# Performance work log

Measured on AMD Instinct MI355X. Metric: run time of the kernel, lower is better.

The kernel has to match this reference:

```python
import jax, jax.numpy as jnp
import numpy as np

EPS = 1e-6
HEADS = 16

def _ln(x):
    m = jnp.mean(x, axis=-1, keepdims=True)
    v = jnp.mean((x - m) ** 2, axis=-1, keepdims=True)
    return (x - m) / jnp.sqrt(v + EPS)

def _modulate(x, shift, scale):
    # shift/scale: [B,T,D] broadcast over H,W
    return x * (1.0 + scale[:, :, None, None, :]) + shift[:, :, None, None, :]

def _gate(x, g):
    return x * g[:, :, None, None, :]

def _mlp(x, w1, b1, w2, b2):
    h = jax.nn.gelu(x @ w1 + b1, approximate=True)
    return h @ w2 + b2

def _attn(tokens, qkv_w, out_w, out_b, causal):
    # tokens: [N, L, D]
    N, L, D = tokens.shape
    dh = D // HEADS
    qkv = tokens @ qkv_w  # [N, L, 3D]
    q, k, v = jnp.split(qkv, 3, axis=-1)
    q = q.reshape(N, L, HEADS, dh)
    k = k.reshape(N, L, HEADS, dh)
    v = v.reshape(N, L, HEADS, dh)
    scores = jnp.einsum('nqhd,nkhd->nhqk', q, k) * (1.0 / np.sqrt(dh))
    if causal:
        mask = jnp.tril(jnp.ones((L, L), dtype=bool))
        scores = jnp.where(mask, scores, jnp.finfo(scores.dtype).min)
    p = jax.nn.softmax(scores, axis=-1)
    o = jnp.einsum('nhqk,nkhd->nqhd', p, v).reshape(N, L, D)
    return o @ out_w + out_b

def _lstm(xseq, w_ih, w_hh, b_ih, b_hh):
    # xseq: [N, T, D]; PyTorch gate order i,f,g,o; zero initial state
    N = xseq.shape[0]
    Hh = w_hh.shape[0]
    def step(carry, xt):
        h, cc = carry
        gates = xt @ w_ih + h @ w_hh + (b_ih + b_hh)  # [N, 4H]
        i, f, g, o = jnp.split(gates, 4, axis=-1)
        cc = jax.nn.sigmoid(f) * cc + jax.nn.sigmoid(i) * jnp.tanh(g)
        h = jax.nn.sigmoid(o) * jnp.tanh(cc)
        return (h, cc), h
    h0 = jnp.zeros((N, Hh), xseq.dtype)
    (_, _), ys = jax.lax.scan(step, (h0, h0), jnp.swapaxes(xseq, 0, 1))
    return jnp.swapaxes(ys, 0, 1)

def _forward(x, c, s_ada_w, s_ada_b, t_ada_w, t_ada_b, r_ada_w, r_ada_b,
             s_qkv_w, s_out_w, s_out_b, t_qkv_w, t_out_w, t_out_b,
             s_mlp_w1, s_mlp_b1, s_mlp_w2, s_mlp_b2,
             t_mlp_w1, t_mlp_b1, t_mlp_w2, t_mlp_b2,
             lstm_w_ih, lstm_w_hh, lstm_b_ih, lstm_b_hh):
    B, T, H, W, D = x.shape
    cs = jax.nn.silu(c)
    s_mod = jnp.split(cs @ s_ada_w + s_ada_b, 6, axis=-1)
    s_shift_msa, s_scale_msa, s_gate_msa, s_shift_mlp, s_scale_mlp, s_gate_mlp = s_mod
    # spatial attention over (H*W) tokens, per (B,T)
    h1 = _modulate(_ln(x), s_shift_msa, s_scale_msa)
    a = _attn(h1.reshape(B * T, H * W, D), s_qkv_w, s_out_w, s_out_b, causal=False)
    x = x + _gate(a.reshape(B, T, H, W, D), s_gate_msa)
    x = x + _gate(_mlp(_modulate(_ln(x), s_shift_mlp, s_scale_mlp), s_mlp_w1, s_mlp_b1, s_mlp_w2, s_mlp_b2), s_gate_mlp)
    t_mod = jnp.split(cs @ t_ada_w + t_ada_b, 6, axis=-1)
    t_shift_msa, t_scale_msa, t_gate_msa, t_shift_mlp, t_scale_mlp, t_gate_mlp = t_mod
    # temporal causal attention over T, per (B,H,W)
    h2 = _modulate(_ln(x), t_shift_msa, t_scale_msa)
    tok = jnp.transpose(h2, (0, 2, 3, 1, 4)).reshape(B * H * W, T, D)
    a = _attn(tok, t_qkv_w, t_out_w, t_out_b, causal=True)
    a = jnp.transpose(a.reshape(B, H, W, T, D), (0, 3, 1, 2, 4))
    x = x + _gate(a, t_gate_msa)
    x = x + _gate(_mlp(_modulate(_ln(x), t_shift_mlp, t_scale_mlp), t_mlp_w1, t_mlp_b1, t_mlp_w2, t_mlp_b2), t_gate_mlp)
    # recurrent branch: LSTM over T per spatial token
    r_shift, r_scale, r_gate = jnp.split(cs @ r_ada_w + r_ada_b, 3, axis=-1)
    residual = x
    xr = _modulate(_ln(x), r_shift, r_scale)
    xr = jnp.transpose(xr, (0, 2, 3, 1, 4)).reshape(B * H * W, T, D)
    out = _lstm(xr, lstm_w_ih, lstm_w_hh, lstm_b_ih, lstm_b_hh)
    out = jnp.transpose(out.reshape(B, H, W, T, D), (0, 3, 1, 2, 4))
    return residual + _gate(out, r_gate)

def setup_inputs() -> dict:
    key = jax.random.key(0)
    ks = jax.random.split(key, 24)
    B, T, H, W, D = 2, 16, 16, 16, 1024
    Dff = 4 * D
    s = 0.02
    inp = {}
    inp['x'] = jax.random.normal(ks[0], (B, T, H, W, D), jnp.float32)
    inp['c'] = jax.random.normal(ks[1], (B, T, D), jnp.float32)
    inp['s_ada_w'] = jax.random.normal(ks[2], (D, 6 * D), jnp.float32) * s
    inp['s_ada_b'] = jnp.zeros((6 * D,), jnp.float32)
    inp['t_ada_w'] = jax.random.normal(ks[3], (D, 6 * D), jnp.float32) * s
    inp['t_ada_b'] = jnp.zeros((6 * D,), jnp.float32)
    inp['r_ada_w'] = jax.random.normal(ks[4], (D, 3 * D), jnp.float32) * s
    inp['r_ada_b'] = jnp.zeros((3 * D,), jnp.float32)
    inp['s_qkv_w'] = jax.random.normal(ks[5], (D, 3 * D), jnp.float32) * s
    inp['s_out_w'] = jax.random.normal(ks[6], (D, D), jnp.float32) * s
    inp['s_out_b'] = jnp.zeros((D,), jnp.float32)
    inp['t_qkv_w'] = jax.random.normal(ks[7], (D, 3 * D), jnp.float32) * s
    inp['t_out_w'] = jax.random.normal(ks[8], (D, D), jnp.float32) * s
    inp['t_out_b'] = jnp.zeros((D,), jnp.float32)
    inp['s_mlp_w1'] = jax.random.normal(ks[9], (D, Dff), jnp.float32) * s
    inp['s_mlp_b1'] = jnp.zeros((Dff,), jnp.float32)
    inp['s_mlp_w2'] = jax.random.normal(ks[10], (Dff, D), jnp.float32) * s
    inp['s_mlp_b2'] = jnp.zeros((D,), jnp.float32)
    inp['t_mlp_w1'] = jax.random.normal(ks[11], (D, Dff), jnp.float32) * s
    inp['t_mlp_b1'] = jnp.zeros((Dff,), jnp.float32)
    inp['t_mlp_w2'] = jax.random.normal(ks[12], (Dff, D), jnp.float32) * s
    inp['t_mlp_b2'] = jnp.zeros((D,), jnp.float32)
    inp['lstm_w_ih'] = jax.random.normal(ks[13], (D, 4 * D), jnp.float32) * s
    inp['lstm_w_hh'] = jax.random.normal(ks[14], (D, 4 * D), jnp.float32) * s
    inp['lstm_b_ih'] = jnp.zeros((4 * D,), jnp.float32)
    inp['lstm_b_hh'] = jnp.zeros((4 * D,), jnp.float32)
    return inp

def reference(x, c, s_ada_w, s_ada_b, t_ada_w, t_ada_b, r_ada_w, r_ada_b,
              s_qkv_w, s_out_w, s_out_b, t_qkv_w, t_out_w, t_out_b,
              s_mlp_w1, s_mlp_b1, s_mlp_w2, s_mlp_b2,
              t_mlp_w1, t_mlp_b1, t_mlp_w2, t_mlp_b2,
              lstm_w_ih, lstm_w_hh, lstm_b_ih, lstm_b_hh):
    return _forward(x, c, s_ada_w, s_ada_b, t_ada_w, t_ada_b, r_ada_w, r_ada_b,
                    s_qkv_w, s_out_w, s_out_b, t_qkv_w, t_out_w, t_out_b,
                    s_mlp_w1, s_mlp_b1, s_mlp_w2, s_mlp_b2,
                    t_mlp_w1, t_mlp_b1, t_mlp_w2, t_mlp_b2,
                    lstm_w_ih, lstm_w_hh, lstm_b_ih, lstm_b_hh)
```

## Files before the change

### kernel.cpp

```cpp
#include <hip/hip_runtime.h>
#include <hip/hip_bf16.h>
#include <stdint.h>

typedef unsigned short u16;
typedef unsigned int u32;
typedef short short8 __attribute__((ext_vector_type(8)));
typedef float f32x4 __attribute__((ext_vector_type(4)));

#define SBAR()   __builtin_amdgcn_s_barrier()
#define WAITV(n) asm volatile("s_waitcnt vmcnt(" #n ")")
#define WAITL0() asm volatile("s_waitcnt lgkmcnt(0)")

__device__ __forceinline__ float bl(u32 x){ return __uint_as_float(x<<16); }
__device__ __forceinline__ float bh(u32 x){ return __uint_as_float(x & 0xffff0000u); }
__device__ __forceinline__ float b2f(u16 x){ return __uint_as_float(((u32)x)<<16); }
__device__ __forceinline__ u16 f2b(float f){
  u32 u = __float_as_uint(f);
  u32 r = (u + 0x7fffu + ((u>>16)&1u)) >> 16;
  return (u16)r;
}
__device__ __forceinline__ u32 pk2(float a, float b){ return (u32)f2b(a) | ((u32)f2b(b)<<16); }
__device__ __forceinline__ float tanh_f(float x){ return 1.f - 2.f/(__expf(2.f*x)+1.f); }
__device__ __forceinline__ float sigm(float x){ return 1.f/(1.f+__expf(-x)); }
__device__ __forceinline__ float gelu_t(float x){
  float u = 0.7978845608028654f*(x + 0.044715f*x*x*x);
  return 0.5f*x*(1.f + tanh_f(u));
}
__device__ __forceinline__ void gld_lds16(const u16* g, u16* lds_base){
  __builtin_amdgcn_global_load_lds((const __attribute__((address_space(1))) void*)g,
                                   (__attribute__((address_space(3))) void*)lds_base,
                                   16, 0, 0);
}

__global__ void transpose_f2b(const float* __restrict__ in, u16* __restrict__ out, int R, int C){
  __shared__ u16 t[32][33];
  int c0 = blockIdx.x*32, r0 = blockIdx.y*32;
  int tx = threadIdx.x, ty = threadIdx.y;
  #pragma unroll
  for (int i=0;i<4;++i) t[ty+i*8][tx] = f2b(in[(size_t)(r0+ty+i*8)*C + c0+tx]);
  __syncthreads();
  #pragma unroll
  for (int i=0;i<4;++i) out[(size_t)(c0+ty+i*8)*R + r0+tx] = t[tx][ty+i*8];
}

__global__ void silu_k(const float* __restrict__ c, float* __restrict__ cs){
  int i = blockIdx.x*256 + threadIdx.x;
  float v = c[i];
  cs[i] = v * sigm(v);
}

__global__ void add_bias(const float* __restrict__ a, const float* __restrict__ b,
                         float* __restrict__ o){
  int i = blockIdx.x*256 + threadIdx.x;
  o[i] = a[i] + b[i];
}

__global__ void mod_init(const float* __restrict__ b, float* __restrict__ out, int Nw){
  int j = blockIdx.x*256 + threadIdx.x;
  out[(size_t)blockIdx.y*Nw + j] = b[j];
}
__global__ __launch_bounds__(256)
void mod_part(const float* __restrict__ cs, const float* __restrict__ W,
              float* __restrict__ out, int Nw){
  int j  = blockIdx.x*256 + threadIdx.x;
  int k0 = blockIdx.y*256;
  __shared__ float csl[32*256];
  #pragma unroll
  for (int r=0;r<32;++r) csl[r*256 + threadIdx.x] = cs[(size_t)r*1024 + k0 + threadIdx.x];
  __syncthreads();
  float acc[32];
  #pragma unroll
  for (int r=0;r<32;++r) acc[r] = 0.f;
  for (int k=0;k<256;++k){
    float wv = W[(size_t)(k0+k)*Nw + j];
    #pragma unroll
    for (int r=0;r<32;++r) acc[r] += csl[r*256+k]*wv;
  }
  #pragma unroll
  for (int r=0;r<32;++r) atomicAdd(&out[(size_t)r*Nw + j], acc[r]);
}

__global__ __launch_bounds__(256)
void ln_first(const float* __restrict__ xin, float* __restrict__ xf,
              const float* __restrict__ mod, int stride, int shift_off, int scale_off,
              u16* __restrict__ out){
  int tok = blockIdx.x, tid = threadIdx.x;
  float4 v = *(const float4*)(xin + (size_t)tok*1024 + tid*4);
  *(float4*)(xf + (size_t)tok*1024 + tid*4) = v;
  __shared__ float r1[256], r2[256];
  r1[tid] = v.x+v.y+v.z+v.w;
  r2[tid] = v.x*v.x+v.y*v.y+v.z*v.z+v.w*v.w;
  __syncthreads();
  for (int off=128; off>0; off>>=1){
    if (tid < off){ r1[tid] += r1[tid+off]; r2[tid] += r2[tid+off]; }
    __syncthreads();
  }
  float mean = r1[0]*(1.f/1024.f);
  float var  = r2[0]*(1.f/1024.f) - mean*mean;
  float rstd = rsqrtf(fmaxf(var,0.f) + 1e-6f);
  int bt = tok >> 8;
  const float* mr = mod + (size_t)bt*stride;
  int d = tid*4;
  float4 sh = *(const float4*)(mr + shift_off + d);
  float4 sc = *(const float4*)(mr + scale_off + d);
  float y0 = (v.x-mean)*rstd*(1.f+sc.x)+sh.x;
  float y1 = (v.y-mean)*rstd*(1.f+sc.y)+sh.y;
  float y2 = (v.z-mean)*rstd*(1.f+sc.z)+sh.z;
  float y3 = (v.w-mean)*rstd*(1.f+sc.w)+sh.w;
  uint2 ub; ub.x = pk2(y0,y1); ub.y = pk2(y2,y3);
  *(uint2*)(out + (size_t)tok*1024 + d) = ub;
}

__global__ __launch_bounds__(256)
void gate_ln(float* __restrict__ xf, const u16* __restrict__ o,
             const float* __restrict__ gmod, int gstride, int goff, int gperm,
             const float* __restrict__ lmod, int lstride, int shift_off, int scale_off,
             u16* __restrict__ out, int lperm){
  int tok = blockIdx.x, tid = threadIdx.x;
  int bt = tok >> 8;
  size_t stok = tok;
  if (gperm){ int b=tok>>12, t=(tok>>8)&15, ss=tok&255; stok = ((size_t)(b*256+ss)*16 + t); }
  int d = tid*4;
  uint2 u = *(const uint2*)(o + stok*1024 + d);
  float4 g = *(const float4*)(gmod + (size_t)bt*gstride + goff + d);
  float* xp = xf + (size_t)tok*1024 + d;
  float4 v = *(float4*)xp;
  v.x += bl(u.x)*g.x; v.y += bh(u.x)*g.y; v.z += bl(u.y)*g.z; v.w += bh(u.y)*g.w;
  *(float4*)xp = v;
  __shared__ float r1[256], r2[256];
  r1[tid] = v.x+v.y+v.z+v.w;
  r2[tid] = v.x*v.x+v.y*v.y+v.z*v.z+v.w*v.w;
  __syncthreads();
  for (int off=128; off>0; off>>=1){
    if (tid < off){ r1[tid] += r1[tid+off]; r2[tid] += r2[tid+off]; }
    __syncthreads();
  }
  float mean = r1[0]*(1.f/1024.f);
  float var  = r2[0]*(1.f/1024.f) - mean*mean;
  float rstd = rsqrtf(fmaxf(var,0.f) + 1e-6f);
  const float* mr = lmod + (size_t)bt*lstride;
  float4 sh = *(const float4*)(mr + shift_off + d);
  float4 sc = *(const float4*)(mr + scale_off + d);
  size_t otok = tok;
  if (lperm){ int b=tok>>12, t=(tok>>8)&15, ss=tok&255; otok = ((size_t)(b*256+ss)*16 + t); }
  float y0 = (v.x-mean)*rstd*(1.f+sc.x)+sh.x;
  float y1 = (v.y-mean)*rstd*(1.f+sc.y)+sh.y;
  float y2 = (v.z-mean)*rstd*(1.f+sc.z)+sh.z;
  float y3 = (v.w-mean)*rstd*(1.f+sc.w)+sh.w;
  uint2 ub; ub.x = pk2(y0,y1); ub.y = pk2(y2,y3);
  *(uint2*)(out + otok*1024 + d) = ub;
}

template<int KIND>
__global__ __launch_bounds__(256, 2)
void gemm_nt(const u16* __restrict__ A, const u16* __restrict__ BT,
             u16* __restrict__ outb, float* __restrict__ outf,
             const float* __restrict__ biasf,
             const u16* __restrict__ addend, long astr,
             int M, int N, int K){
  __shared__ u16 As[128*32];
  __shared__ u16 Bs[128*32];
  const int tid  = threadIdx.x;
  const int wid  = tid >> 6, lane = tid & 63;
  const int l16  = lane & 15, quad = lane >> 4;
  const int wm   = wid >> 1,  wn   = wid & 1;
  const int m0   = blockIdx.y * 128, n0 = blockIdx.x * 128;
  f32x4 acc[4][4];
  #pragma unroll
  for (int i=0;i<4;++i)
    #pragma unroll
    for (int j=0;j<4;++j) acc[i][j] = (f32x4){0.f,0.f,0.f,0.f};

  for (int kt = 0; kt < K; kt += 32){
    __syncthreads();
    #pragma unroll
    for (int r = 0; r < 2; ++r){
      int flat = r*256 + wid*64 + lane;
      int row  = flat >> 2;
      int sc   = ((flat & 3) ^ ((row >> 1) & 3)) << 3;
      gld_lds16(&A [(size_t)(m0+row)*K + kt + sc], &As[(size_t)(r*256 + wid*64)*8]);
      gld_lds16(&BT[(size_t)(n0+row)*K + kt + sc], &Bs[(size_t)(r*256 + wid*64)*8]);
    }
    __syncthreads();
    short8 af[4], bfr[4];
    #pragma unroll
    for (int i=0;i<4;++i){
      int row = wm*64+i*16+l16;
      af[i]  = *(const short8*)&As[row*32 + ((quad ^ ((row>>1)&3))<<3)];
    }
    #pragma unroll
    for (int j=0;j<4;++j){
      int row = wn*64+j*16+l16;
      bfr[j] = *(const short8*)&Bs[row*32 + ((quad ^ ((row>>1)&3))<<3)];
    }
    #pragma unroll
    for (int i=0;i<4;++i)
      #pragma unroll
      for (int j=0;j<4;++j)
        acc[i][j] = __builtin_amdgcn_mfma_f32_16x16x32_bf16(af[i], bfr[j], acc[i][j], 0,0,0);
  }
  #pragma unroll
  for (int j=0;j<4;++j){
    int col = n0 + wn*64 + j*16 + l16;
    float bias = 0.f;
    if (KIND==1 || KIND==2) bias = biasf[col];
    #pragma unroll
    for (int i=0;i<4;++i){
      #pragma unroll
      for (int r=0;r<4;++r){
        int row = m0 + wm*64 + i*16 + quad*4 + r;
        float v = acc[i][j][r];
        if (KIND==1||KIND==2) v += bias;
        if (KIND==2) v = gelu_t(v);
        if (KIND==3){
          v += b2f(addend[(size_t)row*astr + col]);
          outf[(size_t)row*N + col] = v;
        } else {
          outb[(size_t)row*N + col] = f2b(v);
        }
      }
    }
  }
}

template<int KIND>
__global__ __launch_bounds__(512, 2)
void gemm256(const u16* __restrict__ A, const u16* __restrict__ BT,
             u16* __restrict__ outb, const float* __restrict__ biasf,
             int M, int N, int K){
  __shared__ u16 S[4][2][256*32];
  const int tid  = threadIdx.x;
  const int wid  = tid >> 6, lane = tid & 63;
  const int l16  = lane & 15, quad = lane >> 4;
  const int wm   = wid >> 2,  wn   = wid & 3;
  const int m0   = blockIdx.y * 256, n0 = blockIdx.x * 256;
  const int NT   = K >> 5;

  f32x4 acc[8][4];
  #pragma unroll
  for (int i=0;i<8;++i)
    #pragma unroll
    for (int j=0;j<4;++j) acc[i][j] = (f32x4){0.f,0.f,0.f,0.f};

  const int f0  = tid,        r0s = f0 >> 2;
  const int f1  = 512 + tid,  r1s = f1 >> 2;
  const int c0s = ((f0 & 3) ^ ((r0s >> 1) & 3)) << 3;
  const int c1s = ((f1 & 3) ^ ((r1s >> 1) & 3)) << 3;
  const int ld0 = (wid*64)*8;
  const int ld1 = (512 + wid*64)*8;

  auto stageA = [&](int t){
    int b = t & 3, kt = t << 5;
    gld_lds16(&A[(size_t)(m0 + r0s)*K + kt + c0s], &S[b][0][ld0]);
    gld_lds16(&A[(size_t)(m0 + r1s)*K + kt + c1s], &S[b][0][ld1]);
  };
  auto stageB = [&](int t){
    int b = t & 3, kt = t << 5;
    gld_lds16(&BT[(size_t)(n0 + r0s)*K + kt + c0s], &S[b][1][ld0]);
    gld_lds16(&BT[(size_t)(n0 + r1s)*K + kt + c1s], &S[b][1][ld1]);
  };

  const int npre = NT < 3 ? NT : 3;
  for (int t=0; t<npre; ++t){ stageA(t); stageB(t); }
  if (NT >= 3)      { WAITV(8); }
  else if (NT == 2) { WAITV(4); }
  else              { WAITV(0); }
  SBAR();

  for (int t=0; t<NT; ++t){
    const int b = t & 3;
    const u16* Ab = &S[b][0][0];
    const u16* Bb = &S[b][1][0];
    short8 afr[4], bfr[4];
    #pragma unroll
    for (int i=0;i<4;++i){
      int row = wm*128 + i*16 + l16;
      afr[i] = *(const short8*)&Ab[row*32 + ((quad ^ ((row>>1)&3))<<3)];
    }
    #pragma unroll
    for (int j=0;j<4;++j){
      int row = wn*64 + j*16 + l16;
      bfr[j] = *(const short8*)&Bb[row*32 + ((quad ^ ((row>>1)&3))<<3)];
    }
    if (t + 3 < NT) stageA(t+3);
    SBAR();
    WAITL0();
    __builtin_amdgcn_s_setprio(1);
    #pragma unroll
    for (int i=0;i<4;++i)
      #pragma unroll
      for (int j=0;j<4;++j)
        acc[i][j] = __builtin_amdgcn_mfma_f32_16x16x32_bf16(afr[i], bfr[j], acc[i][j], 0,0,0);
    __builtin_amdgcn_s_setprio(0);
    SBAR();
    short8 af2[4];
    #pragma unroll
    for (int i=0;i<4;++i){
      int row = wm*128 + (i+4)*16 + l16;
      af2[i] = *(const short8*)&Ab[row*32 + ((quad ^ ((row>>1)&3))<<3)];
    }
    if (t + 3 < NT) stageB(t+3);
    SBAR();
    WAITL0();
    __builtin_amdgcn_s_setprio(1);
    #pragma unroll
    for (int i=0;i<4;++i)
      #pragma unroll
      for (int j=0;j<4;++j)
        acc[i+4][j] = __builtin_amdgcn_mfma_f32_16x16x32_bf16(af2[i], bfr[j], acc[i+4][j], 0,0,0);
    __builtin_amdgcn_s_setprio(0);
    if (t + 3 < NT)      { WAITV(8); }
    else if (t + 2 < NT) { WAITV(4); }
    else if (t + 1 < NT) { WAITV(0); }
    SBAR();
  }

  #pragma unroll
  for (int j=0;j<4;++j){
    int col = n0 + wn*64 + j*16 + l16;
    float bias = 0.f;
    if (KIND==1 || KIND==2) bias = biasf[col];
    #pragma unroll
    for (int i=0;i<8;++i){
      #pragma unroll
      for (int r=0;r<4;++r){
        int row = m0 + wm*128 + i*16 + quad*4 + r;
        float v = acc[i][j][r];
        if (KIND==1||KIND==2) v += bias;
        if (KIND==2) v = gelu_t(v);
        outb[(size_t)row*N + col] = f2b(v);
      }
    }
  }
}

__global__ __launch_bounds__(256)
void attn_spatial_mfma(const u16* __restrict__ qkv, u16* __restrict__ out){
  constexpr int PAD = 80;
  __shared__ u16 Ks[64*PAD];
  __shared__ u16 Vt[64*PAD];
  __shared__ u16 Ps[4*64*PAD];
  int h = blockIdx.x, n = blockIdx.y;
  int tid = threadIdx.x, wid = tid>>6, lane = tid&63, l16 = lane&15, quad = lane>>4;
  u16* Pw = Ps + wid*64*PAD;
  int qrow_base = n*256 + wid*64;
  short8 qf[4][2];
  #pragma unroll
  for (int i=0;i<4;++i)
    #pragma unroll
    for (int c=0;c<2;++c)
      qf[i][c] = *(const short8*)(qkv + (size_t)(qrow_base + i*16 + l16)*3072 + h*64 + c*32 + quad*8);
  f32x4 Oc[4][4];
  float mrun[4][4], lrun[4][4];
  #pragma unroll
  for (int i=0;i<4;++i)
    #pragma unroll
    for (int j=0;j<4;++j){ Oc[i][j] = (f32x4){0.f,0.f,0.f,0.f}; mrun[i][j] = -30000.f; lrun[i][j] = 0.f; }

  for (int kt=0; kt<4; ++kt){
    __syncthreads();
    #pragma unroll
    for (int r=0;r<2;++r){
      int flat = tid + r*256;
      int row = flat>>3, c8 = (flat&7)<<3;
      const u16* kp = qkv + (size_t)(n*256 + kt*64 + row)*3072 + 1024 + h*64 + c8;
      *(short8*)&Ks[row*PAD + c8] = *(const short8*)kp;
      short8 vv = *(const short8*)(kp + 1024);
      #pragma unroll
      for (int j=0;j<8;++j) Vt[(c8+j)*PAD + row] = ((const u16*)&vv)[j];
    }
    __syncthreads();
    f32x4 S[4][4];
    #pragma unroll
    for (int i=0;i<4;++i)
      #pragma unroll
      for (int jt=0;jt<4;++jt) S[i][jt] = (f32x4){0.f,0.f,0.f,0.f};
    #pragma unroll
    for (int c=0;c<2;++c){
      short8 kf[4];
      #pragma unroll
      for (int jt=0;jt<4;++jt) kf[jt] = *(const short8*)&Ks[(jt*16+l16)*PAD + c*32 + quad*8];
      #pragma unroll
      for (int i=0;i<4;++i)
        #pragma unroll
        for (int jt=0;jt<4;++jt)
          S[i][jt] = __builtin_amdgcn_mfma_f32_16x16x32_bf16(qf[i][c], kf[jt], S[i][jt], 0,0,0);
    }
    #pragma unroll
    for (int i=0;i<4;++i){
      #pragma unroll
      for (int r=0;r<4;++r){
        float rm = -30000.f;
        #pragma unroll
        for (int jt=0;jt<4;++jt){ S[i][jt][r] *= 0.125f; rm = fmaxf(rm, S[i][jt][r]); }
        #pragma unroll
        for (int off=1; off<16; off<<=1) rm = fmaxf(rm, __shfl_xor(rm, off));
        float mnew  = fmaxf(mrun[i][r], rm);
        float alpha = __expf(mrun[i][r] - mnew);
        mrun[i][r] = mnew;
        float ps = 0.f;
        #pragma unroll
        for (int jt=0;jt<4;++jt){ float pv = __expf(S[i][jt][r] - mnew); S[i][jt][r] = pv; ps += pv; }
        #pragma unroll
        for (int off=1; off<16; off<<=1) ps += __shfl_xor(ps, off);
        lrun[i][r] = lrun[i][r]*alpha + ps;
        #pragma unroll
        for (int dt=0;dt<4;++dt) Oc[i][dt][r] *= alpha;
        #pragma unroll
        for (int jt=0;jt<4;++jt) Pw[(i*16+quad*4+r)*PAD + jt*16 + l16] = f2b(S[i][jt][r]);
      }
    }
    #pragma unroll
    for (int c=0;c<2;++c){
      short8 pf[4], vf[4];
      #pragma unroll
      for (int i=0;i<4;++i)  pf[i]  = *(const short8*)&Pw[(i*16+l16)*PAD + c*32 + quad*8];
      #pragma unroll
      for (int dt=0;dt<4;++dt) vf[dt] = *(const short8*)&Vt[(dt*16+l16)*PAD + c*32 + quad*8];
      #pragma unroll
      for (int i=0;i<4;++i)
        #pragma unroll
        for (int dt=0;dt<4;++dt)
          Oc[i][dt] = __builtin_amdgcn_mfma_f32_16x16x32_bf16(pf[i], vf[dt], Oc[i][dt], 0,0,0);
    }
  }
  #pragma unroll
  for (int i=0;i<4;++i)
    #pragma unroll
    for (int r=0;r<4;++r){
      float rl = 1.f/lrun[i][r];
      int tok = qrow_base + i*16 + quad*4 + r;
      #pragma unroll
      for (int dt=0;dt<4;++dt)
        out[(size_t)tok*1024 + h*64 + dt*16 + l16] = f2b(Oc[i][dt][r]*rl);
    }
}

__global__ __launch_bounds__(256, 2)
void attn_temporal(const u16* __restrict__ qkv, u16* __restrict__ out){
  int n = blockIdx.x;
  int tid = threadIdx.x;
  int h = tid>>4, q = tid&15;
  __shared__ u16 KV[16*2048];
  #pragma unroll
  for (int i=0;i<16;++i){
    int u4i = tid + i*256;
    int e = u4i*8;
    int t = e>>11, cc = e&2047;
    *(uint4*)&KV[t*2048 + cc] = *(const uint4*)(qkv + ((size_t)(n*16+t)*3072 + 1024 + cc));
  }
  __syncthreads();
  float qr[64];
  const u16* qp = qkv + ((size_t)(n*16+q)*3072 + h*64);
  #pragma unroll
  for (int i=0;i<8;++i){
    uint4 u = *(const uint4*)(qp + i*8);
    qr[i*8+0]=bl(u.x)*0.125f; qr[i*8+1]=bh(u.x)*0.125f;
    qr[i*8+2]=bl(u.y)*0.125f; qr[i*8+3]=bh(u.y)*0.125f;
    qr[i*8+4]=bl(u.z)*0.125f; qr[i*8+5]=bh(u.z)*0.125f;
    qr[i*8+6]=bl(u.w)*0.125f; qr[i*8+7]=bh(u.w)*0.125f;
  }
  float sc[16]; float m = -30000.f;
  #pragma unroll
  for (int kv=0; kv<16; ++kv){
    const uint4* kr = (const uint4*)&KV[kv*2048 + h*64];
    float s = 0.f;
    #pragma unroll
    for (int i=0;i<8;++i){
      uint4 u = kr[i];
      s += qr[i*8+0]*bl(u.x) + qr[i*8+1]*bh(u.x) + qr[i*8+2]*bl(u.y) + qr[i*8+3]*bh(u.y)
         + qr[i*8+4]*bl(u.z) + qr[i*8+5]*bh(u.z) + qr[i*8+6]*bl(u.w) + qr[i*8+7]*bh(u.w);
    }
    s = (kv<=q) ? s : -30000.f;
    sc[kv]=s; m = fmaxf(m,s);
  }
  float l=0.f, acc[64];
  #pragma unroll
  for (int d=0;d<64;++d) acc[d]=0.f;
  #pragma unroll
  for (int kv=0; kv<16; ++kv){
    float p = __expf(sc[kv]-m);
    l += p;
    const uint4* vr = (const uint4*)&KV[kv*2048 + 1024 + h*64];
    #pragma unroll
    for (int i=0;i<8;++i){
      uint4 u = vr[i];
      acc[i*8+0]+=p*bl(u.x); acc[i*8+1]+=p*bh(u.x); acc[i*8+2]+=p*bl(u.y); acc[i*8+3]+=p*bh(u.y);
      acc[i*8+4]+=p*bl(u.z); acc[i*8+5]+=p*bh(u.z); acc[i*8+6]+=p*bl(u.w); acc[i*8+7]+=p*bh(u.w);
    }
  }
  float rl = 1.f/l;
  u16* op = out + ((size_t)(n*16+q)*1024 + h*64);
  #pragma unroll
  for (int i=0;i<8;++i){
    uint4 ub;
    ub.x = pk2(acc[i*8+0]*rl, acc[i*8+1]*rl);
    ub.y = pk2(acc[i*8+2]*rl, acc[i*8+3]*rl);
    ub.z = pk2(acc[i*8+4]*rl, acc[i*8+5]*rl);
    ub.w = pk2(acc[i*8+6]*rl, acc[i*8+7]*rl);
    *(uint4*)(op + i*8) = ub;
  }
}

__global__ void lstm_point(const float* __restrict__ g4, float* __restrict__ cst,
                           u16* __restrict__ hst, u16* __restrict__ hout, int t){
  size_t i4 = ((size_t)blockIdx.x*256 + threadIdx.x)*4;
  int nn = (int)(i4 >> 10);
  int d  = (int)(i4 & 1023);
  const float* g = g4 + (size_t)nn*4096 + d;
  float4 gi = *(const float4*)(g);
  float4 gf = *(const float4*)(g+1024);
  float4 gg = *(const float4*)(g+2048);
  float4 go = *(const float4*)(g+3072);
  float4 c = *(float4*)(cst + i4);
  c.x = sigm(gf.x)*c.x + sigm(gi.x)*tanh_f(gg.x);
  c.y = sigm(gf.y)*c.y + sigm(gi.y)*tanh_f(gg.y);
  c.z = sigm(gf.z)*c.z + sigm(gi.z)*tanh_f(gg.z);
  c.w = sigm(gf.w)*c.w + sigm(gi.w)*tanh_f(gg.w);
  float h0 = sigm(go.x)*tanh_f(c.x);
  float h1 = sigm(go.y)*tanh_f(c.y);
  float h2 = sigm(go.z)*tanh_f(c.z);
  float h3 = sigm(go.w)*tanh_f(c.w);
  *(float4*)(cst + i4) = c;
  uint2 hb; hb.x = pk2(h0,h1); hb.y = pk2(h2,h3);
  *(uint2*)(hst + i4) = hb;
  *(uint2*)(hout + ((size_t)nn*16 + t)*1024 + d) = hb;
}

__global__ void final_out(const float* __restrict__ xf, const u16* __restrict__ hout,
                          const float* __restrict__ rmod, float* __restrict__ out){
  size_t i4 = ((size_t)blockIdx.x*256 + threadIdx.x)*4;
  int tok = (int)(i4>>10), d = (int)(i4&1023);
  int bt = tok>>8;
  int b=tok>>12, t=(tok>>8)&15, ss=tok&255;
  size_t src = (((size_t)(b*256+ss)*16 + t)*1024) + d;
  uint2 u = *(const uint2*)(hout + src);
  float4 g = *(const float4*)(rmod + (size_t)bt*3072 + 2048 + d);
  float4 x = *(const float4*)(xf + i4);
  float4 o;
  o.x = x.x + bl(u.x)*g.x; o.y = x.y + bh(u.x)*g.y;
  o.z = x.z + bl(u.y)*g.z; o.w = x.w + bh(u.y)*g.w;
  *(float4*)(out + i4) = o;
}

extern "C" void kernel_launch(void* const* d_in, const int* in_sizes, int n_in,
                              void* d_out, int out_size, void* d_ws, size_t ws_size,
                              hipStream_t stream){
  (void)in_sizes; (void)n_in; (void)out_size; (void)ws_size;
  const float* x       = (const float*)d_in[0];
  const float* c       = (const float*)d_in[1];
  const float* s_ada_w = (const float*)d_in[2];
  const float* s_ada_b = (const float*)d_in[3];
  const float* t_ada_w = (const float*)d_in[4];
  const float* t_ada_b = (const float*)d_in[5];
  const float* r_ada_w = (const float*)d_in[6];
  const float* r_ada_b = (const float*)d_in[7];
  const float* s_qkv_w = (const float*)d_in[8];
  const float* s_out_w = (const float*)d_in[9];
  const float* s_out_b = (const float*)d_in[10];
  const float* t_qkv_w = (const float*)d_in[11];
  const float* t_out_w = (const float*)d_in[12];
  const float* t_out_b = (const float*)d_in[13];
  const float* s_mlp_w1= (const float*)d_in[14];
  const float* s_mlp_b1= (const float*)d_in[15];
  const float* s_mlp_w2= (const float*)d_in[16];
  const float* s_mlp_b2= (const float*)d_in[17];
  const float* t_mlp_w1= (const float*)d_in[18];
  const float* t_mlp_b1= (const float*)d_in[19];
  const float* t_mlp_w2= (const float*)d_in[20];
  const float* t_mlp_b2= (const float*)d_in[21];
  const float* w_ih    = (const float*)d_in[22];
  const float* w_hh    = (const float*)d_in[23];
  const float* b_ih    = (const float*)d_in[24];
  const float* b_hh    = (const float*)d_in[25];

  char* p = (char*)d_ws;
  auto alloc = [&](size_t sz){ void* r = (void*)p; p += (sz + 255) & ~(size_t)255; return r; };
  float* xf    = (float*)alloc(8192ull*1024*4);
  u16*   h16   = (u16*)  alloc(8192ull*1024*2);
  u16*   big   = (u16*)  alloc(8192ull*4096*2);
  u16*   o16   = (u16*)  alloc(8192ull*1024*2);
  float* gates = (float*)alloc(512ull*4096*4);
  float* cst   = (float*)alloc(512ull*1024*4);
  u16*   hst   = (u16*)  alloc(512ull*1024*2);
  float* cs    = (float*)alloc(32ull*1024*4);
  float* smod  = (float*)alloc(32ull*6144*4);
  float* tmod  = (float*)alloc(32ull*6144*4);
  float* rmod  = (float*)alloc(32ull*3072*4);
  u16*   wT    = (u16*)  alloc(4096ull*1024*2);
  u16*   whhT  = (u16*)  alloc(4096ull*1024*2);
  float* bihh  = (float*)alloc(4096*4);

  dim3 tb(32,8);
  auto T = [&](const float* in, u16* out, int R, int C){
    transpose_f2b<<<dim3(C/32, R/32), tb, 0, stream>>>(in, out, R, C);
  };
  auto GEMM = [&](int kind, const u16* A, const u16* BT, void* out,
                  const float* b1, const u16* add, long astr, int M, int N, int K){
    dim3 g(N/128, M/128);
    switch(kind){
      case 0: gemm_nt<0><<<g,256,0,stream>>>(A,BT,(u16*)out,nullptr,nullptr,nullptr,0,M,N,K); break;
      case 1: gemm_nt<1><<<g,256,0,stream>>>(A,BT,(u16*)out,nullptr,b1,nullptr,0,M,N,K); break;
      case 2: gemm_nt<2><<<g,256,0,stream>>>(A,BT,(u16*)out,nullptr,b1,nullptr,0,M,N,K); break;
      case 3: gemm_nt<3><<<g,256,0,stream>>>(A,BT,nullptr,(float*)out,nullptr,add,astr,M,N,K); break;
    }
  };
  auto GEMM256 = [&](int kind, const u16* A, const u16* BT, u16* out,
                     const float* b1, int M, int N, int K){
    dim3 g(N/256, M/256);
    switch(kind){
      case 0: gemm256<0><<<g,512,0,stream>>>(A,BT,out,nullptr,M,N,K); break;
      case 1: gemm256<1><<<g,512,0,stream>>>(A,BT,out,b1,M,N,K); break;
      case 2: gemm256<2><<<g,512,0,stream>>>(A,BT,out,b1,M,N,K); break;
    }
  };
  auto MOD = [&](const float* W, const float* b, float* out, int Nw){
    mod_init<<<dim3(Nw/256,32),256,0,stream>>>(b, out, Nw);
    mod_part<<<dim3(Nw/256,4),256,0,stream>>>(cs, W, out, Nw);
  };

  silu_k<<<128,256,0,stream>>>(c, cs);
  MOD(s_ada_w, s_ada_b, smod, 6144);
  MOD(t_ada_w, t_ada_b, tmod, 6144);
  MOD(r_ada_w, r_ada_b, rmod, 3072);
  add_bias<<<16,256,0,stream>>>(b_ih, b_hh, bihh);

  ln_first<<<8192,256,0,stream>>>(x, xf, smod, 6144, 0, 1024, h16);
  T(s_qkv_w, wT, 1024, 3072);
  GEMM256(0, h16, wT, big, nullptr, 8192, 3072, 1024);
  attn_spatial_mfma<<<dim3(16,32),256,0,stream>>>(big, h16);
  T(s_out_w, wT, 1024, 1024);
  GEMM(1, h16, wT, o16, s_out_b, nullptr, 0, 8192, 1024, 1024);
  gate_ln<<<8192,256,0,stream>>>(xf, o16, smod, 6144, 2048, 0, smod, 6144, 3072, 4096, h16, 0);
  T(s_mlp_w1, wT, 1024, 4096);
  GEMM256(2, h16, wT, big, s_mlp_b1, 8192, 4096, 1024);
  T(s_mlp_w2, wT, 4096, 1024);
  GEMM(1, big, wT, o16, s_mlp_b2, nullptr, 0, 8192, 1024, 4096);
  gate_ln<<<8192,256,0,stream>>>(xf, o16, smod, 6144, 5120, 0, tmod, 6144, 0, 1024, h16, 1);
  T(t_qkv_w, wT, 1024, 3072);
  GEMM256(0, h16, wT, big, nullptr, 8192, 3072, 1024);
  attn_temporal<<<512,256,0,stream>>>(big, h16);
  T(t_out_w, wT, 1024, 1024);
  GEMM(1, h16, wT, o16, t_out_b, nullptr, 0, 8192, 1024, 1024);
  gate_ln<<<8192,256,0,stream>>>(xf, o16, tmod, 6144, 2048, 1, tmod, 6144, 3072, 4096, h16, 0);
  T(t_mlp_w1, wT, 1024, 4096);
  GEMM256(2, h16, wT, big, t_mlp_b1, 8192, 4096, 1024);
  T(t_mlp_w2, wT, 4096, 1024);
  GEMM(1, big, wT, o16, t_mlp_b2, nullptr, 0, 8192, 1024, 4096);
  gate_ln<<<8192,256,0,stream>>>(xf, o16, tmod, 6144, 5120, 0, rmod, 3072, 0, 1024, h16, 1);
  T(w_ih, wT, 1024, 4096);
  GEMM256(1, h16, wT, big, bihh, 8192, 4096, 1024);
  T(w_hh, whhT, 1024, 4096);
  hipMemsetAsync(cst, 0, 512ull*1024*4, stream);
  hipMemsetAsync(hst, 0, 512ull*1024*2, stream);
  for (int t=0; t<16; ++t){
    GEMM(3, hst, whhT, gates, nullptr, big + (size_t)t*4096, 16*4096, 512, 4096, 1024);
    lstm_point<<<512,256,0,stream>>>(gates, cst, hst, o16, t);
  }
  final_out<<<8192,256,0,stream>>>(xf, o16, rmod, (float*)d_out);
}
```

Baseline: 1.978 ms.

## Simplify GEMM main loop to one barrier per k-tile and reorder epilogue stores

The GEMM main loop drops its two-phase split, which used several barriers and explicit lgkmcnt waits per k-tile. It now issues the prefetch of both A and B for tile t+3 at the start of each iteration, then interleaves A-fragment LDS reads with MFMAs across all 8 row blocks. The goal is to cut barrier and wait overhead and let the compiler overlap LDS reads with MFMA. The epilogue loads bias once into registers and writes in row-major order. The risk is less explicit control over LDS and MFMA interleaving and more register pressure or stalls on LDS reads.

```diff
diff --git a/kernel.cpp b/kernel.cpp
--- a/kernel.cpp
+++ b/kernel.cpp
@@ -9,7 +9,6 @@
 
 #define SBAR()   __builtin_amdgcn_s_barrier()
 #define WAITV(n) asm volatile("s_waitcnt vmcnt(" #n ")")
-#define WAITL0() asm volatile("s_waitcnt lgkmcnt(0)")
 
 __device__ __forceinline__ float bl(u32 x){ return __uint_as_float(x<<16); }
 __device__ __forceinline__ float bh(u32 x){ return __uint_as_float(x & 0xffff0000u); }
@@ -271,43 +270,22 @@
     const int b = t & 3;
     const u16* Ab = &S[b][0][0];
     const u16* Bb = &S[b][1][0];
-    short8 afr[4], bfr[4];
-    #pragma unroll
-    for (int i=0;i<4;++i){
-      int row = wm*128 + i*16 + l16;
-      afr[i] = *(const short8*)&Ab[row*32 + ((quad ^ ((row>>1)&3))<<3)];
-    }
+    if (t + 3 < NT){ stageA(t+3); stageB(t+3); }
+    short8 bfr[4];
     #pragma unroll
     for (int j=0;j<4;++j){
       int row = wn*64 + j*16 + l16;
       bfr[j] = *(const short8*)&Bb[row*32 + ((quad ^ ((row>>1)&3))<<3)];
     }
-    if (t + 3 < NT) stageA(t+3);
-    SBAR();
-    WAITL0();
     __builtin_amdgcn_s_setprio(1);
     #pragma unroll
-    for (int i=0;i<4;++i)
+    for (int i=0;i<8;++i){
+      int row = wm*128 + i*16 + l16;
+      short8 af = *(const short8*)&Ab[row*32 + ((quad ^ ((row>>1)&3))<<3)];
       #pragma unroll
       for (int j=0;j<4;++j)
-        acc[i][j] = __builtin_amdgcn_mfma_f32_16x16x32_bf16(afr[i], bfr[j], acc[i][j], 0,0,0);
-    __builtin_amdgcn_s_setprio(0);
-    SBAR();
-    short8 af2[4];
-    #pragma unroll
-    for (int i=0;i<4;++i){
-      int row = wm*128 + (i+4)*16 + l16;
-      af2[i] = *(const short8*)&Ab[row*32 + ((quad ^ ((row>>1)&3))<<3)];
-    }
-    if (t + 3 < NT) stageB(t+3);
-    SBAR();
-    WAITL0();
-    __builtin_amdgcn_s_setprio(1);
-    #pragma unroll
-    for (int i=0;i<4;++i)
-      #pragma unroll
-      for (int j=0;j<4;++j)
-        acc[i+4][j] = __builtin_amdgcn_mfma_f32_16x16x32_bf16(af2[i], bfr[j], acc[i+4][j], 0,0,0);
+        acc[i][j] = __builtin_amdgcn_mfma_f32_16x16x32_bf16(af, bfr[j], acc[i][j], 0,0,0);
+    }
     __builtin_amdgcn_s_setprio(0);
     if (t + 3 < NT)      { WAITV(8); }
     else if (t + 2 < NT) { WAITV(4); }
@@ -315,18 +293,21 @@
     SBAR();
   }
 
-  #pragma unroll
-  for (int j=0;j<4;++j){
-    int col = n0 + wn*64 + j*16 + l16;
-    float bias = 0.f;
-    if (KIND==1 || KIND==2) bias = biasf[col];
-    #pragma unroll
-    for (int i=0;i<8;++i){
-      #pragma unroll
-      for (int r=0;r<4;++r){
-        int row = m0 + wm*128 + i*16 + quad*4 + r;
+  float biasv[4];
+  if (KIND==1 || KIND==2){
+    #pragma unroll
+    for (int j=0;j<4;++j) biasv[j] = biasf[n0 + wn*64 + j*16 + l16];
+  }
+  #pragma unroll
+  for (int i=0;i<8;++i){
+    #pragma unroll
+    for (int r=0;r<4;++r){
+      int row = m0 + wm*128 + i*16 + quad*4 + r;
+      #pragma unroll
+      for (int j=0;j<4;++j){
+        int col = n0 + wn*64 + j*16 + l16;
         float v = acc[i][j][r];
-        if (KIND==1||KIND==2) v += bias;
+        if (KIND==1||KIND==2) v += biasv[j];
         if (KIND==2) v = gelu_t(v);
         outb[(size_t)row*N + col] = f2b(v);
       }
```

After: 1.911 ms. -3.4%, faster.
